# Performance work log

Hardware: AMD Instinct MI355X
Metric: run time of the kernel (lower is better)

The kernel has to match this reference:

```python
import jax, jax.numpy as jnp
import numpy as np

HEADS, HID, OUT_C, IN_C = 8, 128, 2, 64
D = HID // HEADS
NODE = {"cell0": 50000, "cell1": 100000, "cell2": 25000}
# (src_type, dst_type, edge_name, num_edges)
ETYPES = [("cell0", "cell0", "u00", 200000),
          ("cell1", "cell1", "u11", 200000),
          ("cell1", "cell0", "b10", 100000),
          ("cell2", "cell1", "b21", 50000)]


def _segment_softmax(scores, seg, num_segments):
    # numerically-stable softmax over irregular destination segments
    m = jax.ops.segment_max(scores, seg, num_segments=num_segments)
    e = jnp.exp(scores - m[seg])
    s = jax.ops.segment_sum(e, seg, num_segments=num_segments)
    return e / (s[seg] + 1e-16)


def setup_inputs() -> dict:
    key = jax.random.key(0)
    ks = iter(jax.random.split(key, 64))
    s = 0.1
    inp = {}
    for nt, n in NODE.items():
        inp[f"x_{nt}"] = jax.random.normal(next(ks), (n, IN_C), jnp.float32)
    for st, dt, name, e in ETYPES:
        src = jax.random.randint(next(ks), (e,), 0, NODE[st], jnp.int32)
        dst = jax.random.randint(next(ks), (e,), 0, NODE[dt], jnp.int32)
        inp[f"ei_{name}"] = jnp.stack([src, dst])
    # HANConv params: per node-type projection, per edge-type attention vectors
    for nt in NODE:
        inp[f"W_{nt}"] = jax.random.normal(next(ks), (IN_C, HID), jnp.float32) * s
        inp[f"b_{nt}"] = jnp.zeros((HID,), jnp.float32)
    for _, _, name, _ in ETYPES:
        inp[f"as_{name}"] = jax.random.normal(next(ks), (HEADS, D), jnp.float32) * s
        inp[f"ad_{name}"] = jax.random.normal(next(ks), (HEADS, D), jnp.float32) * s
    # semantic attention params + final classifier
    inp["k_w"] = jax.random.normal(next(ks), (HID, HID), jnp.float32) * s
    inp["k_b"] = jnp.zeros((HID,), jnp.float32)
    inp["q"] = jax.random.normal(next(ks), (HID,), jnp.float32) * s
    inp["lin_w"] = jax.random.normal(next(ks), (HID, OUT_C), jnp.float32) * s
    inp["lin_b"] = jnp.zeros((OUT_C,), jnp.float32)
    return inp


def _han_conv(x, ei, W, b, att_s, att_d, k_w, k_b, q):
    # node-level: project each node type -> [N, H, D]
    h = {nt: (x[nt] @ W[nt] + b[nt]).reshape(-1, HEADS, D) for nt in NODE}
    outs = {nt: [] for nt in NODE}
    for st, dt, name, _ in ETYPES:
        xs, xd = h[st], h[dt]
        a_s = (xs * att_s[name]).sum(-1)  # [Ns, H]
        a_d = (xd * att_d[name]).sum(-1)  # [Nd, H]
        src, dst = ei[name][0], ei[name][1]
        alpha = jax.nn.leaky_relu(a_s[src] + a_d[dst], 0.2)  # [E, H]
        alpha = _segment_softmax(alpha, dst, NODE[dt])
        msg = xs[src] * alpha[:, :, None]  # [E, H, D]
        agg = jax.ops.segment_sum(msg, dst, num_segments=NODE[dt])
        outs[dt].append(jax.nn.relu(agg.reshape(-1, HID)))
    # semantic-level attention across metapaths per dst node type
    res = {}
    for nt, lst in outs.items():
        if not lst:
            res[nt] = None
            continue
        stk = jnp.stack(lst)  # [M, N, HID]
        score = (q * jnp.tanh(stk @ k_w + k_b).mean(1)).sum(-1)  # [M]
        attn = jax.nn.softmax(score)
        res[nt] = jnp.einsum('m,mnf->nf', attn, stk)
    return res


def reference(x_cell0, x_cell1, x_cell2,
              W_cell0, b_cell0, W_cell1, b_cell1, W_cell2, b_cell2,
              as_u00, ad_u00, as_u11, ad_u11, as_b10, ad_b10, as_b21, ad_b21,
              k_w, k_b, q, lin_w, lin_b,
              ei_u00, ei_u11, ei_b10, ei_b21):
    x = {"cell0": x_cell0, "cell1": x_cell1, "cell2": x_cell2}
    ei = {"u00": ei_u00, "u11": ei_u11, "b10": ei_b10, "b21": ei_b21}
    W = {"cell0": W_cell0, "cell1": W_cell1, "cell2": W_cell2}
    b = {"cell0": b_cell0, "cell1": b_cell1, "cell2": b_cell2}
    att_s = {"u00": as_u00, "u11": as_u11, "b10": as_b10, "b21": as_b21}
    att_d = {"u00": ad_u00, "u11": ad_u11, "b10": ad_b10, "b21": ad_b21}
    # HAN.forward calls han_conv twice with identical inputs (first result
    # discarded); in eval mode (dropout off) both calls are identical math,
    # so we compute it once.
    out = _han_conv(x, ei, W, b, att_s, att_d, k_w, k_b, q)
    pooled = sum(jnp.sum(v, axis=0) for v in out.values() if v is not None)  # global_add_pool, batch=None
    return jax.nn.sigmoid(pooled[None, :] @ lin_w + lin_b)  # [1, OUT_C]
```

## Files before the change

kernel.cpp:

```cpp
#include <hip/hip_runtime.h>
#include <hip/hip_fp16.h>

#define N0 50000
#define N1 100000
#define N2 25000
#define E00 200000
#define E11 200000
#define E10 100000
#define E21 50000
#define EE  550000
#define ND  300000
#define NB  293
#define NT_ALL 18750
#define HID 128
#define INC 64

typedef _Float16 half8 __attribute__((ext_vector_type(8)));
typedef _Float16 half4_t __attribute__((ext_vector_type(4)));
typedef float float4v __attribute__((ext_vector_type(4)));
typedef float floatx2 __attribute__((ext_vector_type(2)));

struct PrepT {
    const float* W; const float* bias;
    const float* av0; const float* av1; const float* av2; const float* av3;
    _Float16* wtg; _Float16* adtg; float* bdc;
};

__device__ __forceinline__ void decode_edge(
    int e, const int* ei00, const int* ei10, const int* ei11, const int* ei21,
    int& src, int& slot)
{
    if (e < E00)                    { src = ei00[e];               slot = ei00[E00 + e]; }
    else if (e < E00 + E10)         { int i = e - E00;             src = ei10[i]; slot = 50000  + ei10[E10 + i]; }
    else if (e < E00 + E10 + E11)   { int i = e - E00 - E10;       src = ei11[i]; slot = 100000 + ei11[E11 + i]; }
    else                            { int i = e - E00 - E10 - E11; src = ei21[i]; slot = 200000 + ei21[E21 + i]; }
}

__global__ __launch_bounds__(256) void prep_kernel(
    PrepT p0, PrepT p1, PrepT p2,
    const float* __restrict__ kw, const float* __restrict__ lw,
    unsigned char* __restrict__ kwf8,
    const int* __restrict__ ei00, const int* __restrict__ ei10,
    const int* __restrict__ ei11, const int* __restrict__ ei21,
    int* __restrict__ cnt)
{
    if (blockIdx.x >= 32) {
        int e = (blockIdx.x - 32) * 256 + threadIdx.x;
        if (e >= EE) return;
        int src, slot;
        decode_edge(e, ei00, ei10, ei11, ei21, src, slot);
        atomicAdd(&cnt[slot], 1);
        return;
    }
    if (blockIdx.x >= 24) {
        int base = (blockIdx.x - 24) * 256 + threadIdx.x;
        for (int it = 0; it < 9; ++it) {
            int idx = base + it * 2048;
            int f = idx >> 7, g = idx & 127;
            float v;
            if (f < 128)      v = 2.0f * kw[g * 128 + f];
            else if (f < 130) v = lw[g * 2 + (f - 128)];
            else              v = 0.f;
            int r = __builtin_amdgcn_cvt_pk_fp8_f32(v, 0.f, 0, false);
            kwf8[idx] = (unsigned char)r;
        }
        return;
    }
    PrepT P = (blockIdx.x >= 16) ? p2 : (blockIdx.x >= 8) ? p1 : p0;
    const int lb = blockIdx.x & 7;
    const int t2 = lb * 256 + threadIdx.x;
    {
        int f = t2 >> 4, g0 = (t2 & 15) * 4;
        half4_t v;
#pragma unroll
        for (int j = 0; j < 4; ++j) v[j] = (_Float16)P.W[(g0 + j) * 128 + f];
        *(half4_t*)&P.wtg[f * 64 + g0] = v;
    }
    {
        int c = t2 >> 6, g = t2 & 63;
        const float* av = (c < 8) ? P.av0 : (c < 16) ? P.av1 : (c < 24) ? P.av2 : P.av3;
        float v = 0.f;
        if (av) {
            int hh = c & 7;
#pragma unroll
            for (int d = 0; d < 16; ++d)
                v += P.W[g * 128 + hh * 16 + d] * av[hh * 16 + d];
        }
        P.adtg[c * 64 + g] = (_Float16)v;
    }
    if (lb == 0 && threadIdx.x < 32) {
        int c = threadIdx.x;
        const float* av = (c < 8) ? P.av0 : (c < 16) ? P.av1 : (c < 24) ? P.av2 : P.av3;
        float v = 0.f;
        if (av) {
            int hh = c & 7;
#pragma unroll
            for (int d = 0; d < 16; ++d)
                v += P.bias[hh * 16 + d] * av[hh * 16 + d];
        }
        P.bdc[c] = v;
    }
}

struct PT {
    const float* x; const float* bias; unsigned char* h;
    _Float16* ao0; _Float16* ao1; _Float16* ao2; _Float16* ao3;
    const _Float16* wtg; const _Float16* adtg; const float* bdc;
    int N; int ntiles; int bstart; int nblocks;
};

#define HPAD 136
#define PROJ_BLKS 1024

__global__ __launch_bounds__(256, 2) void proj_mfma(
    PT t0, PT t1, PT t2,
    const int* __restrict__ cnt, int* __restrict__ part)
{
    __shared__ _Float16 ht[4][16][HPAD];
    __shared__ int swt[4];
    const int tid = threadIdx.x;
    const int lane = tid & 63, wv = tid >> 6;
    const int fi = lane & 15, hi = lane >> 4;

    if (blockIdx.x >= PROJ_BLKS) {
        const int b = blockIdx.x - PROJ_BLKS;
        int i0 = b * 1024 + tid * 4;
        int s = 0;
#pragma unroll
        for (int k = 0; k < 4; ++k) { int i = i0 + k; s += (i < ND) ? cnt[i] : 0; }
#pragma unroll
        for (int off = 1; off < 64; off <<= 1) s += __shfl_xor(s, off);
        if ((tid & 63) == 0) swt[tid >> 6] = s;
        __syncthreads();
        if (tid == 0) part[b] = swt[0] + swt[1] + swt[2] + swt[3];
        return;
    }

    PT A = (blockIdx.x >= t2.bstart) ? t2 : (blockIdx.x >= t1.bstart) ? t1 : t0;

    half8 bfr[8][2], bd[2][2];
#pragma unroll
    for (int nt = 0; nt < 8; ++nt)
#pragma unroll
        for (int kb = 0; kb < 2; ++kb)
            bfr[nt][kb] = *(const half8*)&A.wtg[(nt * 16 + fi) * 64 + kb * 32 + hi * 8];
#pragma unroll
    for (int t = 0; t < 2; ++t)
#pragma unroll
        for (int kb = 0; kb < 2; ++kb)
            bd[t][kb] = *(const half8*)&A.adtg[(t * 16 + fi) * 64 + kb * 32 + hi * 8];

    float bvv[8];
#pragma unroll
    for (int nt = 0; nt < 8; ++nt) bvv[nt] = A.bias[nt * 16 + fi];
    const float bdc0 = A.bdc[fi];
    const float bdc1 = A.bdc[16 + fi];

    _Float16* aolo = (fi >= 8) ? A.ao1 : A.ao0;
    _Float16* aohi = (fi >= 8) ? A.ao3 : A.ao2;
    const bool has_hi = (A.ao2 != nullptr) || (A.ao3 != nullptr);

    const int stride = A.nblocks * 4;
    int t = (blockIdx.x - A.bstart) * 4 + wv;
    float4 u0, u1, u2, u3;
    if (t < A.ntiles) {
        int rsrc = t * 16 + fi; if (rsrc >= A.N) rsrc = A.N - 1;
        const float* xp = A.x + (size_t)rsrc * 64 + hi * 8;
        u0 = *(const float4*)(xp);
        u1 = *(const float4*)(xp + 4);
        u2 = *(const float4*)(xp + 32);
        u3 = *(const float4*)(xp + 36);
    }
    for (; t < A.ntiles; ) {
        const int tn = t + stride;
        float4 n0, n1, n2, n3;
        if (tn < A.ntiles) {
            int rsrc = tn * 16 + fi; if (rsrc >= A.N) rsrc = A.N - 1;
            const float* xp = A.x + (size_t)rsrc * 64 + hi * 8;
            n0 = *(const float4*)(xp);
            n1 = *(const float4*)(xp + 4);
            n2 = *(const float4*)(xp + 32);
            n3 = *(const float4*)(xp + 36);
        }
        const int base = t * 16;
        half8 a0, a1;
        a0[0] = (_Float16)u0.x; a0[1] = (_Float16)u0.y; a0[2] = (_Float16)u0.z; a0[3] = (_Float16)u0.w;
        a0[4] = (_Float16)u1.x; a0[5] = (_Float16)u1.y; a0[6] = (_Float16)u1.z; a0[7] = (_Float16)u1.w;
        a1[0] = (_Float16)u2.x; a1[1] = (_Float16)u2.y; a1[2] = (_Float16)u2.z; a1[3] = (_Float16)u2.w;
        a1[4] = (_Float16)u3.x; a1[5] = (_Float16)u3.y; a1[6] = (_Float16)u3.z; a1[7] = (_Float16)u3.w;

        float4v c[8];
#pragma unroll
        for (int nt = 0; nt < 8; ++nt) {
            float4v z = {0.f, 0.f, 0.f, 0.f};
            z = __builtin_amdgcn_mfma_f32_16x16x32_f16(a0, bfr[nt][0], z, 0, 0, 0);
            z = __builtin_amdgcn_mfma_f32_16x16x32_f16(a1, bfr[nt][1], z, 0, 0, 0);
            c[nt] = z;
        }
        float4v d0 = {0.f, 0.f, 0.f, 0.f};
        d0 = __builtin_amdgcn_mfma_f32_16x16x32_f16(a0, bd[0][0], d0, 0, 0, 0);
        d0 = __builtin_amdgcn_mfma_f32_16x16x32_f16(a1, bd[0][1], d0, 0, 0, 0);
        float4v d1 = {0.f, 0.f, 0.f, 0.f};
        if (has_hi) {
            d1 = __builtin_amdgcn_mfma_f32_16x16x32_f16(a0, bd[1][0], d1, 0, 0, 0);
            d1 = __builtin_amdgcn_mfma_f32_16x16x32_f16(a1, bd[1][1], d1, 0, 0, 0);
        }

#pragma unroll
        for (int nt = 0; nt < 8; ++nt)
#pragma unroll
            for (int r = 0; r < 4; ++r)
                ht[wv][hi * 4 + r][nt * 16 + fi] = (_Float16)(c[nt][r] + bvv[nt]);
#pragma unroll
        for (int i = 0; i < 4; ++i) {
            int row = i * 4 + hi;
            int node = base + row;
            if (node < A.N) {
                half8 v = *(const half8*)&ht[wv][row][fi * 8];
                int pa = __builtin_amdgcn_cvt_pk_fp8_f32((float)v[0], (float)v[1], 0, false);
                pa = __builtin_amdgcn_cvt_pk_fp8_f32((float)v[2], (float)v[3], pa, true);
                int pb = __builtin_amdgcn_cvt_pk_fp8_f32((float)v[4], (float)v[5], 0, false);
                pb = __builtin_amdgcn_cvt_pk_fp8_f32((float)v[6], (float)v[7], pb, true);
                int2 o = {pa, pb};
                *(int2*)(A.h + (size_t)node * 128 + fi * 8) = o;
            }
        }
        if (aolo) {
#pragma unroll
            for (int r = 0; r < 4; ++r) {
                int node = base + hi * 4 + r;
                if (node < A.N) aolo[(size_t)node * 8 + (fi & 7)] = (_Float16)(d0[r] + bdc0);
            }
        }
        if (aohi) {
#pragma unroll
            for (int r = 0; r < 4; ++r) {
                int node = base + hi * 4 + r;
                if (node < A.N) aohi[(size_t)node * 8 + (fi & 7)] = (_Float16)(d1[r] + bdc1);
            }
        }
        t = tn;
        u0 = n0; u1 = n1; u2 = n2; u3 = n3;
    }
}

__global__ __launch_bounds__(256) void scan23_kernel(
    const int* __restrict__ cnt, const int* __restrict__ part,
    int* __restrict__ off, int* __restrict__ cursor)
{
    __shared__ int sd[256];
    __shared__ int pex[512];
    __shared__ int wt[4];
    const int tid = threadIdx.x, b = blockIdx.x;
    const int lane = tid & 63, wv = tid >> 6;

    int p0 = (2 * tid     < NB) ? part[2 * tid]     : 0;
    int p1 = (2 * tid + 1 < NB) ? part[2 * tid + 1] : 0;
    int ps = p0 + p1;
    sd[tid] = ps; __syncthreads();
    for (int d = 1; d < 256; d <<= 1) {
        int v = (tid >= d) ? sd[tid - d] : 0;
        __syncthreads();
        sd[tid] += v;
        __syncthreads();
    }
    int exc = sd[tid] - ps;
    pex[2 * tid] = exc;
    pex[2 * tid + 1] = exc + p0;
    __syncthreads();

    int i0 = b * 1024 + tid * 4;
    int v[4];
#pragma unroll
    for (int k = 0; k < 4; ++k) { int i = i0 + k; v[k] = (i < ND) ? cnt[i] : 0; }
    int ts = v[0] + v[1] + v[2] + v[3];
    int inc = ts;
#pragma unroll
    for (int d = 1; d < 64; d <<= 1) {
        int u = __shfl_up(inc, d);
        if (lane >= d) inc += u;
    }
    int wexc = inc - ts;
    if (lane == 63) wt[wv] = inc;
    __syncthreads();
    int wbase = 0;
    for (int w = 0; w < wv; ++w) wbase += wt[w];
    int base = pex[b] + wbase + wexc;
    int pre = 0;
#pragma unroll
    for (int k = 0; k < 4; ++k) {
        int i = i0 + k;
        if (i < ND) { off[i] = base + pre; cursor[i] = base + pre; }
        pre += v[k];
    }
}

__global__ __launch_bounds__(256) void fill_kernel(
    const int* __restrict__ ei00, const int* __restrict__ ei10,
    const int* __restrict__ ei11, const int* __restrict__ ei21,
    int* __restrict__ cursor, int* __restrict__ srcs)
{
    int e = blockIdx.x * 256 + threadIdx.x;
    if (e >= EE) return;
    int src, slot;
    decode_edge(e, ei00, ei10, ei11, ei21, src, slot);
    int pos = atomicAdd(&cursor[slot], 1);
    srcs[pos] = src;
}

__global__ __launch_bounds__(256) void gather_kernel(
    const int* __restrict__ cnt, const int* __restrict__ off,
    const int* __restrict__ srcs,
    const unsigned char* __restrict__ h0, const unsigned char* __restrict__ h1,
    const unsigned char* __restrict__ h2,
    const _Float16* __restrict__ as00, const _Float16* __restrict__ ad00,
    const _Float16* __restrict__ as10, const _Float16* __restrict__ ad10,
    const _Float16* __restrict__ as11, const _Float16* __restrict__ ad11,
    const _Float16* __restrict__ as21, const _Float16* __restrict__ ad21,
    unsigned char* __restrict__ agg)
{
    const int gid = blockIdx.x * 256 + threadIdx.x;
    const int lane = gid & 63;
    const int g8 = lane >> 3, sub = lane & 7;
    const int slot = (gid >> 6) * 8 + g8;
    const unsigned char* hs;
    const _Float16* asp;
    float adv;
    if (slot < 50000)       { hs = h0; asp = as00; adv = (float)ad00[(size_t)slot * 8 + sub]; }
    else if (slot < 100000) { hs = h1; asp = as10; adv = (float)ad10[(size_t)(slot - 50000) * 8 + sub]; }
    else if (slot < 200000) { hs = h1; asp = as11; adv = (float)ad11[(size_t)(slot - 100000) * 8 + sub]; }
    else                    { hs = h2; asp = as21; adv = (float)ad21[(size_t)(slot - 200000) * 8 + sub]; }
    const int deg = cnt[slot], st = off[slot];

    int degm = deg;
    degm = max(degm, __shfl_xor(degm, 8));
    degm = max(degm, __shfl_xor(degm, 16));
    degm = max(degm, __shfl_xor(degm, 32));

    float acc[16];
#pragma unroll
    for (int j = 0; j < 16; ++j) acc[j] = 0.f;
    float sw = 0.f;

    int i = 0;
    for (; i + 2 <= degm; i += 2) {
        bool a0 = (i < deg), a1 = (i + 1 < deg);
        int s0 = 0, s1 = 0;
        if (a0) s0 = srcs[st + i];
        if (a1) s1 = srcs[st + i + 1];
        float w0 = 0.f, w1 = 0.f;
        int4 v0 = {0, 0, 0, 0}, v1 = {0, 0, 0, 0};
        if (a0) { float v = (float)asp[(size_t)s0 * 8 + sub] + adv;
                  v = v > 0.f ? v : 0.2f * v;
                  w0 = __expf(v);
                  v0 = *(const int4*)(hs + (size_t)s0 * 128 + sub * 16); }
        if (a1) { float v = (float)asp[(size_t)s1 * 8 + sub] + adv;
                  v = v > 0.f ? v : 0.2f * v;
                  w1 = __expf(v);
                  v1 = *(const int4*)(hs + (size_t)s1 * 128 + sub * 16); }
        const int wa[4] = {v0.x, v0.y, v0.z, v0.w};
        const int wb[4] = {v1.x, v1.y, v1.z, v1.w};
#pragma unroll
        for (int k = 0; k < 4; ++k) {
            floatx2 fa0 = __builtin_amdgcn_cvt_pk_f32_fp8(wa[k], false);
            floatx2 fa1 = __builtin_amdgcn_cvt_pk_f32_fp8(wa[k], true);
            floatx2 fb0 = __builtin_amdgcn_cvt_pk_f32_fp8(wb[k], false);
            floatx2 fb1 = __builtin_amdgcn_cvt_pk_f32_fp8(wb[k], true);
            acc[4 * k + 0] += w0 * fa0.x + w1 * fb0.x;
            acc[4 * k + 1] += w0 * fa0.y + w1 * fb0.y;
            acc[4 * k + 2] += w0 * fa1.x + w1 * fb1.x;
            acc[4 * k + 3] += w0 * fa1.y + w1 * fb1.y;
        }
        sw += w0 + w1;
    }
    if (i < degm) {
        bool a0 = (i < deg);
        int s0 = 0;
        if (a0) s0 = srcs[st + i];
        float w0 = 0.f;
        int4 v0 = {0, 0, 0, 0};
        if (a0) { float v = (float)asp[(size_t)s0 * 8 + sub] + adv;
                  v = v > 0.f ? v : 0.2f * v;
                  w0 = __expf(v);
                  v0 = *(const int4*)(hs + (size_t)s0 * 128 + sub * 16); }
        const int wa[4] = {v0.x, v0.y, v0.z, v0.w};
#pragma unroll
        for (int k = 0; k < 4; ++k) {
            floatx2 fa0 = __builtin_amdgcn_cvt_pk_f32_fp8(wa[k], false);
            floatx2 fa1 = __builtin_amdgcn_cvt_pk_f32_fp8(wa[k], true);
            acc[4 * k + 0] += w0 * fa0.x;
            acc[4 * k + 1] += w0 * fa0.y;
            acc[4 * k + 2] += w0 * fa1.x;
            acc[4 * k + 3] += w0 * fa1.y;
        }
        sw += w0;
    }

    float rr = __builtin_amdgcn_rcpf(sw + 1e-16f);
    int4 o;
    int pk[4];
#pragma unroll
    for (int k = 0; k < 4; ++k) {
        float r0 = fmaxf(acc[4 * k + 0] * rr, 0.f);
        float r1 = fmaxf(acc[4 * k + 1] * rr, 0.f);
        float r2 = fmaxf(acc[4 * k + 2] * rr, 0.f);
        float r3 = fmaxf(acc[4 * k + 3] * rr, 0.f);
        int p = __builtin_amdgcn_cvt_pk_fp8_f32(r0, r1, 0, false);
        p = __builtin_amdgcn_cvt_pk_fp8_f32(r2, r3, p, true);
        pk[k] = p;
    }
    o.x = pk[0]; o.y = pk[1]; o.z = pk[2]; o.w = pk[3];
    *(int4*)(agg + (size_t)slot * 128 + sub * 16) = o;
}

__global__ __launch_bounds__(256, 4) void semantic_kernel(
    const unsigned char* __restrict__ agg, const unsigned char* __restrict__ kwf8,
    const float* __restrict__ kb, const float* __restrict__ q,
    const float* __restrict__ lb,
    float* __restrict__ cs2, float* __restrict__ score,
    unsigned int* __restrict__ done, float* __restrict__ out)
{
    __shared__ long lbs[2304];
    __shared__ float kbl[128];
    __shared__ float qla[128];
    __shared__ float redv[12];
    const int tid = threadIdx.x;
    const int lane = tid & 63, wv = tid >> 6;
    const int fi = lane & 15, hi = lane >> 4;

    if (tid < 12) redv[tid] = 0.f;
    for (int it = 0; it < 9; ++it) {
        int e = it * 256 + tid;
        int gk = e >> 6, lp = e & 63;
        int gw = gk >> 2, kkw = gk & 3;
        int fiw = lp & 15, hiw = lp >> 4;
        lbs[e] = *(const long*)&kwf8[(gw * 16 + fiw) * 128 + kkw * 32 + hiw * 8];
    }
    if (tid < 128) kbl[tid] = 2.f * kb[tid];
    else           qla[tid - 128] = 2.f * q[tid - 128];

    const int wid = blockIdx.x * 4 + wv;
    const int nw = gridDim.x * 4;

    long af0[4], af1[4], af2[4], af3[4], af4[4];
#define LOADT(I, AF)                                                            \
    {   const int tt = wid + (I) * nw;                                          \
        if (tt < NT_ALL) {                                                      \
            const unsigned char* rowp = agg + ((size_t)(tt * 16 + fi) * 128 + hi * 8); \
            AF[0] = *(const long*)(rowp);       AF[1] = *(const long*)(rowp + 32); \
            AF[2] = *(const long*)(rowp + 64);  AF[3] = *(const long*)(rowp + 96); \
        } else { AF[0] = 0; AF[1] = 0; AF[2] = 0; AF[3] = 0; } }
    LOADT(0, af0) LOADT(1, af1) LOADT(2, af2) LOADT(3, af3) LOADT(4, af4)

    __syncthreads();

    float c4q = 0.f;
#pragma unroll
    for (int g = 0; g < 8; ++g) c4q += 2.f * qla[g * 16 + fi];

    const long* lbl = lbs + lane;

    float sc[4] = {0.f, 0.f, 0.f, 0.f};
    float cs[4] = {0.f, 0.f, 0.f, 0.f};

#define COMPT(I, AF)                                                            \
    {   const int tt = wid + (I) * nw;                                          \
        if (tt < NT_ALL) {                                                      \
            const int m = (tt >= 12500) ? 3 : (tt >= 6250) ? 2 : (tt >= 3125) ? 1 : 0; \
            float tn0 = 0.f, tn1 = 0.f, tn2 = 0.f, tn3 = 0.f, tcs = 0.f;        \
            _Pragma("unroll 3")                                                 \
            for (int g = 0; g < 9; ++g) {                                       \
                long b0 = lbl[g * 256 + 0];                                     \
                long b1 = lbl[g * 256 + 64];                                    \
                long b2 = lbl[g * 256 + 128];                                   \
                long b3 = lbl[g * 256 + 192];                                   \
                if (g < 8) {                                                    \
                    float kbg = kbl[g * 16 + fi];                               \
                    float qg  = qla[g * 16 + fi];                               \
                    float4v c = {kbg, kbg, kbg, kbg};                           \
                    c = __builtin_amdgcn_mfma_f32_16x16x32_fp8_fp8(AF[0], b0, c, 0, 0, 0); \
                    c = __builtin_amdgcn_mfma_f32_16x16x32_fp8_fp8(AF[1], b1, c, 0, 0, 0); \
                    c = __builtin_amdgcn_mfma_f32_16x16x32_fp8_fp8(AF[2], b2, c, 0, 0, 0); \
                    c = __builtin_amdgcn_mfma_f32_16x16x32_fp8_fp8(AF[3], b3, c, 0, 0, 0); \
                    float e0 = __expf(c[0]); tn0 += qg * __builtin_amdgcn_rcpf(e0 + 1.f); \
                    float e1 = __expf(c[1]); tn1 += qg * __builtin_amdgcn_rcpf(e1 + 1.f); \
                    float e2 = __expf(c[2]); tn2 += qg * __builtin_amdgcn_rcpf(e2 + 1.f); \
                    float e3 = __expf(c[3]); tn3 += qg * __builtin_amdgcn_rcpf(e3 + 1.f); \
                } else {                                                        \
                    float4v c = {0.f, 0.f, 0.f, 0.f};                           \
                    c = __builtin_amdgcn_mfma_f32_16x16x32_fp8_fp8(AF[0], b0, c, 0, 0, 0); \
                    c = __builtin_amdgcn_mfma_f32_16x16x32_fp8_fp8(AF[1], b1, c, 0, 0, 0); \
                    c = __builtin_amdgcn_mfma_f32_16x16x32_fp8_fp8(AF[2], b2, c, 0, 0, 0); \
                    c = __builtin_amdgcn_mfma_f32_16x16x32_fp8_fp8(AF[3], b3, c, 0, 0, 0); \
                    tcs = c[0] + c[1] + c[2] + c[3];                            \
                }                                                               \
            }                                                                   \
            float tsc = c4q - ((tn0 + tn1) + (tn2 + tn3));                      \
            if (m == 0)      { sc[0] += tsc; cs[0] += tcs; }                    \
            else if (m == 1) { sc[1] += tsc; cs[1] += tcs; }                    \
            else if (m == 2) { sc[2] += tsc; cs[2] += tcs; }                    \
            else             { sc[3] += tsc; cs[3] += tcs; }                    \
        } }
    COMPT(0, af0) COMPT(1, af1) COMPT(2, af2) COMPT(3, af3) COMPT(4, af4)

#pragma unroll
    for (int m = 0; m < 4; ++m) {
        float s = sc[m];
#pragma unroll
        for (int off = 1; off < 64; off <<= 1) s += __shfl_xor(s, off);
        if (lane == 0 && s != 0.f) atomicAdd(&redv[m], s);
        float v = cs[m];
        v += __shfl_xor(v, 16);
        v += __shfl_xor(v, 32);
        if (hi == 0 && fi < 2 && v != 0.f) atomicAdd(&redv[4 + 2 * m + fi], v);
    }
    __syncthreads();
    if (tid < 4)              atomicAdd(&score[tid], redv[tid]);
    if (tid >= 4 && tid < 12) atomicAdd(&cs2[tid - 4], redv[tid]);

    __syncthreads();
    if (tid == 0) {
        __threadfence();
        unsigned int old = atomicAdd(done, 1u);
        if (old == gridDim.x - 1) {
            __threadfence();
            float s0 = score[0] / (float)N0;
            float s1 = score[1] / (float)N0;
            float s2 = score[2] / (float)N1;
            float s3 = score[3] / (float)N1;
            float m0 = fmaxf(s0, s1);
            float e0 = __expf(s0 - m0), e1 = __expf(s1 - m0);
            float a0 = e0 / (e0 + e1), a1 = e1 / (e0 + e1);
            float m1 = fmaxf(s2, s3);
            float e2 = __expf(s2 - m1), e3 = __expf(s3 - m1);
            float a2 = e2 / (e2 + e3), a3 = e3 / (e2 + e3);
            float z0 = a0 * cs2[0] + a1 * cs2[2] + a2 * cs2[4] + a3 * cs2[6] + lb[0];
            float z1 = a0 * cs2[1] + a1 * cs2[3] + a2 * cs2[5] + a3 * cs2[7] + lb[1];
            out[0] = 1.f / (1.f + __expf(-z0));
            out[1] = 1.f / (1.f + __expf(-z1));
        }
    }
}

extern "C" void kernel_launch(void* const* d_in, const int* in_sizes, int n_in,
                              void* d_out, int out_size, void* d_ws, size_t ws_size,
                              hipStream_t stream)
{
    const float* x0  = (const float*)d_in[0];
    const float* x1  = (const float*)d_in[1];
    const float* x2  = (const float*)d_in[2];
    const int* ei00  = (const int*)d_in[3];
    const int* ei11  = (const int*)d_in[4];
    const int* ei10  = (const int*)d_in[5];
    const int* ei21  = (const int*)d_in[6];
    const float* W0  = (const float*)d_in[7];  const float* b0 = (const float*)d_in[8];
    const float* W1  = (const float*)d_in[9];  const float* b1 = (const float*)d_in[10];
    const float* W2  = (const float*)d_in[11]; const float* b2 = (const float*)d_in[12];
    const float* as00 = (const float*)d_in[13]; const float* ad00 = (const float*)d_in[14];
    const float* as11 = (const float*)d_in[15]; const float* ad11 = (const float*)d_in[16];
    const float* as10 = (const float*)d_in[17]; const float* ad10 = (const float*)d_in[18];
    const float* as21 = (const float*)d_in[19]; const float* ad21 = (const float*)d_in[20];
    const float* kw  = (const float*)d_in[21]; const float* kb  = (const float*)d_in[22];
    const float* q   = (const float*)d_in[23];
    const float* lw  = (const float*)d_in[24]; const float* lb  = (const float*)d_in[25];
    float* out = (float*)d_out;

    char* p = (char*)d_ws;
    auto alloc = [&](size_t bytes) {
        char* r = p;
        p += (bytes + 255) & ~(size_t)255;
        return r;
    };
    unsigned char* h0 = (unsigned char*)alloc((size_t)N0 * 128);
    unsigned char* h1 = (unsigned char*)alloc((size_t)N1 * 128);
    unsigned char* h2 = (unsigned char*)alloc((size_t)N2 * 128);
    _Float16* o_as00 = (_Float16*)alloc((size_t)N0 * 16);
    _Float16* o_ad00 = (_Float16*)alloc((size_t)N0 * 16);
    _Float16* o_as11 = (_Float16*)alloc((size_t)N1 * 16);
    _Float16* o_ad11 = (_Float16*)alloc((size_t)N1 * 16);
    _Float16* o_as10 = (_Float16*)alloc((size_t)N1 * 16);
    _Float16* o_ad10 = (_Float16*)alloc((size_t)N0 * 16);
    _Float16* o_as21 = (_Float16*)alloc((size_t)N2 * 16);
    _Float16* o_ad21 = (_Float16*)alloc((size_t)N1 * 16);
    int* off    = (int*)alloc((size_t)ND * 4);
    int* cursor = (int*)alloc((size_t)ND * 4);
    int* part   = (int*)alloc((size_t)512 * 4);
    int* srcs   = (int*)alloc((size_t)EE * 4);
    unsigned char* agg = (unsigned char*)alloc((size_t)ND * 128);
    _Float16* wtg0 = (_Float16*)alloc(128 * 64 * 2);
    _Float16* wtg1 = (_Float16*)alloc(128 * 64 * 2);
    _Float16* wtg2 = (_Float16*)alloc(128 * 64 * 2);
    _Float16* adtg0 = (_Float16*)alloc(32 * 64 * 2);
    _Float16* adtg1 = (_Float16*)alloc(32 * 64 * 2);
    _Float16* adtg2 = (_Float16*)alloc(32 * 64 * 2);
    float* bdcg = (float*)alloc(3 * 32 * 4);
    unsigned char* kwf8 = (unsigned char*)alloc(144 * 128);
    char* zstart = p;
    int* cnt = (int*)alloc((size_t)ND * 4);
    float* colsum2 = (float*)alloc(8 * 4);
    float* score   = (float*)alloc(4 * 4);
    unsigned int* done = (unsigned int*)alloc(4);
    size_t zbytes = (size_t)(p - zstart);

    (void)hipMemsetAsync(zstart, 0, zbytes, stream);

    PrepT pp0 = {W0, b0, as00, ad00, ad10, nullptr, wtg0, adtg0, bdcg + 0};
    PrepT pp1 = {W1, b1, as11, ad11, as10, ad21,    wtg1, adtg1, bdcg + 32};
    PrepT pp2 = {W2, b2, as21, nullptr, nullptr, nullptr, wtg2, adtg2, bdcg + 64};
    prep_kernel<<<32 + (EE + 255) / 256, 256, 0, stream>>>(
        pp0, pp1, pp2, kw, lw, kwf8, ei00, ei10, ei11, ei21, cnt);

    PT t0 = {x0, b0, h0,
             o_as00, o_ad00, o_ad10, nullptr,
             wtg0, adtg0, bdcg + 0,
             N0, 3125, 0, 296};
    PT t1 = {x1, b1, h1,
             o_as11, o_ad11, o_as10, o_ad21,
             wtg1, adtg1, bdcg + 32,
             N1, 6250, 296, 584};
    PT t2 = {x2, b2, h2,
             o_as21, nullptr, nullptr, nullptr,
             wtg2, adtg2, bdcg + 64,
             N2, 1563, 880, 144};
    proj_mfma<<<PROJ_BLKS + NB, 256, 0, stream>>>(t0, t1, t2, cnt, part);

    scan23_kernel<<<NB, 256, 0, stream>>>(cnt, part, off, cursor);

    fill_kernel<<<(EE + 255) / 256, 256, 0, stream>>>(ei00, ei10, ei11, ei21,
                                                      cursor, srcs);

    gather_kernel<<<ND / 32, 256, 0, stream>>>(cnt, off, srcs, h0, h1, h2,
        o_as00, o_ad00, o_as10, o_ad10, o_as11, o_ad11, o_as21, o_ad21, agg);

    semantic_kernel<<<1024, 256, 0, stream>>>(agg, kwf8, kb, q, lb,
                                              colsum2, score, done, out);
}
```

Before: 258.7 us.

## Move edge-count atomics into projection launch and prefetch gather source indices

The per-destination edge counting moves out of the tiny prep kernel and into extra blocks of the projection kernel, so the atomics overlap with the MFMA projection work. The block-partial sum of the counts, which needs the counts to be finished, moves into its own small kernel launched afterwards. In the gather loop, the source indices for the next pair of edges are loaded one iteration early to hide index-load latency. This adds a kernel launch and more blocks to the projection grid, and may contend with projection blocks for bandwidth.

```diff
diff --git a/kernel.cpp b/kernel.cpp
--- a/kernel.cpp
+++ b/kernel.cpp
@@ -14,11 +14,22 @@
 #define NT_ALL 18750
 #define HID 128
 #define INC 64
+#define CNT_BLKS 2149
 
 typedef _Float16 half8 __attribute__((ext_vector_type(8)));
 typedef _Float16 half4_t __attribute__((ext_vector_type(4)));
 typedef float float4v __attribute__((ext_vector_type(4)));
 typedef float floatx2 __attribute__((ext_vector_type(2)));
+
+__device__ __forceinline__ void decode_edge(
+    int e, const int* ei00, const int* ei10, const int* ei11, const int* ei21,
+    int& src, int& slot)
+{
+    if (e < E00)                    { src = ei00[e];               slot = ei00[E00 + e]; }
+    else if (e < E00 + E10)         { int i = e - E00;             src = ei10[i]; slot = 50000  + ei10[E10 + i]; }
+    else if (e < E00 + E10 + E11)   { int i = e - E00 - E10;       src = ei11[i]; slot = 100000 + ei11[E11 + i]; }
+    else                            { int i = e - E00 - E10 - E11; src = ei21[i]; slot = 200000 + ei21[E21 + i]; }
+}
 
 struct PrepT {
     const float* W; const float* bias;
@@ -26,32 +37,11 @@
     _Float16* wtg; _Float16* adtg; float* bdc;
 };
 
-__device__ __forceinline__ void decode_edge(
-    int e, const int* ei00, const int* ei10, const int* ei11, const int* ei21,
-    int& src, int& slot)
-{
-    if (e < E00)                    { src = ei00[e];               slot = ei00[E00 + e]; }
-    else if (e < E00 + E10)         { int i = e - E00;             src = ei10[i]; slot = 50000  + ei10[E10 + i]; }
-    else if (e < E00 + E10 + E11)   { int i = e - E00 - E10;       src = ei11[i]; slot = 100000 + ei11[E11 + i]; }
-    else                            { int i = e - E00 - E10 - E11; src = ei21[i]; slot = 200000 + ei21[E21 + i]; }
-}
-
 __global__ __launch_bounds__(256) void prep_kernel(
     PrepT p0, PrepT p1, PrepT p2,
     const float* __restrict__ kw, const float* __restrict__ lw,
-    unsigned char* __restrict__ kwf8,
-    const int* __restrict__ ei00, const int* __restrict__ ei10,
-    const int* __restrict__ ei11, const int* __restrict__ ei21,
-    int* __restrict__ cnt)
-{
-    if (blockIdx.x >= 32) {
-        int e = (blockIdx.x - 32) * 256 + threadIdx.x;
-        if (e >= EE) return;
-        int src, slot;
-        decode_edge(e, ei00, ei10, ei11, ei21, src, slot);
-        atomicAdd(&cnt[slot], 1);
-        return;
-    }
+    unsigned char* __restrict__ kwf8)
+{
     if (blockIdx.x >= 24) {
         int base = (blockIdx.x - 24) * 256 + threadIdx.x;
         for (int it = 0; it < 9; ++it) {
@@ -114,25 +104,21 @@
 
 __global__ __launch_bounds__(256, 2) void proj_mfma(
     PT t0, PT t1, PT t2,
-    const int* __restrict__ cnt, int* __restrict__ part)
+    const int* __restrict__ ei00, const int* __restrict__ ei10,
+    const int* __restrict__ ei11, const int* __restrict__ ei21,
+    int* __restrict__ cnt)
 {
     __shared__ _Float16 ht[4][16][HPAD];
-    __shared__ int swt[4];
     const int tid = threadIdx.x;
     const int lane = tid & 63, wv = tid >> 6;
     const int fi = lane & 15, hi = lane >> 4;
 
     if (blockIdx.x >= PROJ_BLKS) {
-        const int b = blockIdx.x - PROJ_BLKS;
-        int i0 = b * 1024 + tid * 4;
-        int s = 0;
-#pragma unroll
-        for (int k = 0; k < 4; ++k) { int i = i0 + k; s += (i < ND) ? cnt[i] : 0; }
-#pragma unroll
-        for (int off = 1; off < 64; off <<= 1) s += __shfl_xor(s, off);
-        if ((tid & 63) == 0) swt[tid >> 6] = s;
-        __syncthreads();
-        if (tid == 0) part[b] = swt[0] + swt[1] + swt[2] + swt[3];
+        int e = (blockIdx.x - PROJ_BLKS) * 256 + tid;
+        if (e >= EE) return;
+        int src, slot;
+        decode_edge(e, ei00, ei10, ei11, ei21, src, slot);
+        atomicAdd(&cnt[slot], 1);
         return;
     }
 
@@ -244,6 +230,23 @@
     }
 }
 
+__global__ __launch_bounds__(256) void scan1_kernel(
+    const int* __restrict__ cnt, int* __restrict__ part)
+{
+    __shared__ int swt[4];
+    const int tid = threadIdx.x;
+    const int b = blockIdx.x;
+    int i0 = b * 1024 + tid * 4;
+    int s = 0;
+#pragma unroll
+    for (int k = 0; k < 4; ++k) { int i = i0 + k; s += (i < ND) ? cnt[i] : 0; }
+#pragma unroll
+    for (int off = 1; off < 64; off <<= 1) s += __shfl_xor(s, off);
+    if ((tid & 63) == 0) swt[tid >> 6] = s;
+    __syncthreads();
+    if (tid == 0) part[b] = swt[0] + swt[1] + swt[2] + swt[3];
+}
+
 __global__ __launch_bounds__(256) void scan23_kernel(
     const int* __restrict__ cnt, const int* __restrict__ part,
     int* __restrict__ off, int* __restrict__ cursor)
@@ -342,12 +345,19 @@
     for (int j = 0; j < 16; ++j) acc[j] = 0.f;
     float sw = 0.f;
 
+    bool a0n = (0 < deg), a1n = (1 < deg);
+    int s0n = 0, s1n = 0;
+    if (a0n) s0n = srcs[st + 0];
+    if (a1n) s1n = srcs[st + 1];
+
     int i = 0;
     for (; i + 2 <= degm; i += 2) {
-        bool a0 = (i < deg), a1 = (i + 1 < deg);
-        int s0 = 0, s1 = 0;
-        if (a0) s0 = srcs[st + i];
-        if (a1) s1 = srcs[st + i + 1];
+        const bool a0 = a0n, a1 = a1n;
+        const int s0 = s0n, s1 = s1n;
+        a0n = (i + 2 < deg); a1n = (i + 3 < deg);
+        if (a0n) s0n = srcs[st + i + 2];
+        if (a1n) s1n = srcs[st + i + 3];
+
         float w0 = 0.f, w1 = 0.f;
         int4 v0 = {0, 0, 0, 0}, v1 = {0, 0, 0, 0};
         if (a0) { float v = (float)asp[(size_t)s0 * 8 + sub] + adv;
@@ -374,15 +384,12 @@
         sw += w0 + w1;
     }
     if (i < degm) {
-        bool a0 = (i < deg);
-        int s0 = 0;
-        if (a0) s0 = srcs[st + i];
         float w0 = 0.f;
         int4 v0 = {0, 0, 0, 0};
-        if (a0) { float v = (float)asp[(size_t)s0 * 8 + sub] + adv;
-                  v = v > 0.f ? v : 0.2f * v;
-                  w0 = __expf(v);
-                  v0 = *(const int4*)(hs + (size_t)s0 * 128 + sub * 16); }
+        if (a0n) { float v = (float)asp[(size_t)s0n * 8 + sub] + adv;
+                   v = v > 0.f ? v : 0.2f * v;
+                   w0 = __expf(v);
+                   v0 = *(const int4*)(hs + (size_t)s0n * 128 + sub * 16); }
         const int wa[4] = {v0.x, v0.y, v0.z, v0.w};
 #pragma unroll
         for (int k = 0; k < 4; ++k) {
@@ -607,8 +614,7 @@
     PrepT pp0 = {W0, b0, as00, ad00, ad10, nullptr, wtg0, adtg0, bdcg + 0};
     PrepT pp1 = {W1, b1, as11, ad11, as10, ad21,    wtg1, adtg1, bdcg + 32};
     PrepT pp2 = {W2, b2, as21, nullptr, nullptr, nullptr, wtg2, adtg2, bdcg + 64};
-    prep_kernel<<<32 + (EE + 255) / 256, 256, 0, stream>>>(
-        pp0, pp1, pp2, kw, lw, kwf8, ei00, ei10, ei11, ei21, cnt);
+    prep_kernel<<<32, 256, 0, stream>>>(pp0, pp1, pp2, kw, lw, kwf8);
 
     PT t0 = {x0, b0, h0,
              o_as00, o_ad00, o_ad10, nullptr,
@@ -622,7 +628,10 @@
              o_as21, nullptr, nullptr, nullptr,
              wtg2, adtg2, bdcg + 64,
              N2, 1563, 880, 144};
-    proj_mfma<<<PROJ_BLKS + NB, 256, 0, stream>>>(t0, t1, t2, cnt, part);
+    proj_mfma<<<PROJ_BLKS + CNT_BLKS, 256, 0, stream>>>(t0, t1, t2,
+        ei00, ei10, ei11, ei21, cnt);
+
+    scan1_kernel<<<NB, 256, 0, stream>>>(cnt, part);
 
     scan23_kernel<<<NB, 256, 0, stream>>>(cnt, part, off, cursor);
 
```

Result: no change. 258.1 us (-0.2%).
